# Performance work log

Measured on AMD Instinct MI355X. Metric: run time of the kernel, lower is better.

The kernel has to match this reference:

```python
import jax, jax.numpy as jnp
import numpy as np

GRID_SHAPE = (256, 256)  # SOM lattice dims -> M = 65536 nodes, ndim = 2
D = 32                   # input feature dim
B = 2048                 # batch size


def _make_grid_flat():
    # tf.meshgrid(indexing='ij') stacked on last axis, flattened to [1, M, ndim]
    mesh = np.stack(np.meshgrid(*[np.arange(s) for s in GRID_SHAPE], indexing='ij'), axis=-1)
    g = mesh.reshape(1, -1, len(GRID_SHAPE)).astype(np.float32)
    # faithful to source: per-axis mean (reduce_mean axis=1), GLOBAL std (reduce_std, no axis)
    g = (g - g.mean(axis=1, keepdims=True)) / g.std()
    return jnp.asarray(g)


def setup_inputs() -> dict:
    key = jax.random.key(0)
    k1, k2 = jax.random.split(key)
    grid_flat = _make_grid_flat()                                  # [1, M, 2]
    M = grid_flat.shape[1]
    w = jax.random.normal(k1, (1, M, D), dtype=jnp.float32)        # codebook (non-trainable in source)
    x = jax.random.normal(k2, (B, D), dtype=jnp.float32)
    return {"x": x, "grid_flat": grid_flat, "w": w}


def reference(x, grid_flat, w):
    # squared L2 distance from each input to every codebook vector.
    # computed here without materializing the [B, M, D] broadcast.
    wm = w[0]  # [M, D]
    d2 = (jnp.sum(x * x, axis=1, keepdims=True)
          - 2.0 * (x @ wm.T)
          + jnp.sum(wm * wm, axis=1)[None, :])  # [B, M]
    # source: top_k(-|d2|, k=1); d2 >= 0 so abs is identity, kept for fidelity
    _, idx = jax.lax.top_k(-jnp.abs(d2), 1)  # idx: [B, 1]
    bmu = grid_flat[0][idx[:, 0]]            # gather winning grid coords -> [B, 2]
    return bmu
```

## Files before the change

kernel.cpp:

```cpp
#include <hip/hip_runtime.h>
#include <stdint.h>

#define D       32
#define B       2048
#define M       65536
#define STRIPS  1024
#define CHUNKS  4
#define CHCOLS  (B / CHUNKS)
#define NTILES  (CHCOLS / 16)
#define SGROUPS 32
#define SPERG   (STRIPS / SGROUPS)

typedef _Float16 half8 __attribute__((ext_vector_type(8)));
typedef float    floatx4 __attribute__((ext_vector_type(4)));


__global__ void som_wnorm_kernel(const float* __restrict__ w,
                                 float* __restrict__ wnorm) {
    int t   = blockIdx.x * blockDim.x + threadIdx.x;
    int row = t >> 2;
    int j   = t & 3;
    const float4* p = (const float4*)(w + (size_t)row * D) + j * 2;
    float4 a = p[0];
    float4 b4 = p[1];
    float s = a.x * a.x + a.y * a.y + a.z * a.z + a.w * a.w
            + b4.x * b4.x + b4.y * b4.y + b4.z * b4.z + b4.w * b4.w;
    s += __shfl_xor(s, 1);
    s += __shfl_xor(s, 2);
    if (j == 0) wnorm[row] = 0.5f * s;
}

__global__ void split_x_kernel(const float* __restrict__ x,
                               _Float16* __restrict__ xh,
                               _Float16* __restrict__ xl) {
    int i = blockIdx.x * blockDim.x + threadIdx.x;
    float v = x[i];
    _Float16 h = (_Float16)v;
    xh[i] = h;
    xl[i] = (_Float16)(v - (float)h);
}

__global__ __launch_bounds__(256, 4)
void som_mfma_kernel(const float* __restrict__ w,
                     const float* __restrict__ wnorm,
                     const _Float16* __restrict__ x_hi,
                     const _Float16* __restrict__ x_lo,
                     uint64_t* __restrict__ pkeys) {
    const int s    = blockIdx.x;
    const int wv   = threadIdx.x >> 6;
    const int lane = threadIdx.x & 63;
    const int q    = lane >> 4;
    const int j    = lane & 15;

    half8 a_hi[4], a_lo[4];
#pragma unroll
    for (int t = 0; t < 4; t++) {
        const float* wp = w + (size_t)(s * 64 + t * 16 + j) * D + q * 8;
        float4 f0 = ((const float4*)wp)[0];
        float4 f1 = ((const float4*)wp)[1];
        float f[8] = {f0.x, f0.y, f0.z, f0.w, f1.x, f1.y, f1.z, f1.w};
#pragma unroll
        for (int k = 0; k < 8; k++) {
            _Float16 h = (_Float16)f[k];
            a_hi[t][k] = h;
            a_lo[t][k] = (_Float16)(f[k] - (float)h);
        }
    }

    float wn[4][4];
#pragma unroll
    for (int t = 0; t < 4; t++)
#pragma unroll
        for (int r = 0; r < 4; r++)
            wn[t][r] = wnorm[s * 64 + t * 16 + q * 4 + r];

    uint64_t* pk = pkeys + (size_t)s * B;

    for (int it = 0; it < NTILES; it++) {
        const int nb  = wv * CHCOLS + it * 16;
        const int col = nb + j;
        const half8 bh = *(const half8*)(x_hi + (size_t)col * D + q * 8);
        const half8 bl = *(const half8*)(x_lo + (size_t)col * D + q * 8);

        floatx4 acc[4];
#pragma unroll
        for (int t = 0; t < 4; t++)
            acc[t] = __builtin_amdgcn_mfma_f32_16x16x32_f16(
                a_lo[t], bh, (floatx4){0.f, 0.f, 0.f, 0.f}, 0, 0, 0);
#pragma unroll
        for (int t = 0; t < 4; t++)
            acc[t] = __builtin_amdgcn_mfma_f32_16x16x32_f16(a_hi[t], bl, acc[t], 0, 0, 0);
#pragma unroll
        for (int t = 0; t < 4; t++)
            acc[t] = __builtin_amdgcn_mfma_f32_16x16x32_f16(a_hi[t], bh, acc[t], 0, 0, 0);

        float best = -3.4e38f;
        int   brow = 0;
#pragma unroll
        for (int t = 0; t < 4; t++)
#pragma unroll
            for (int r = 0; r < 4; r++) {
                float sc  = acc[t][r] - wn[t][r];
                int   row = s * 64 + t * 16 + q * 4 + r;
                if (sc > best) { best = sc; brow = row; }
            }

        uint32_t u = __float_as_uint(best);
        u ^= (uint32_t)((int32_t)u >> 31) | 0x80000000u;
        uint64_t key = ((uint64_t)u << 32) | (uint64_t)(~(uint32_t)brow);

        uint64_t o;
        o = (uint64_t)__shfl_xor((long long)key, 16); if (o > key) key = o;
        o = (uint64_t)__shfl_xor((long long)key, 32); if (o > key) key = o;

        if (lane < 16) pk[col] = key;
    }
}

__global__ void som_reduce1_kernel(const uint64_t* __restrict__ pkeys,
                                   uint64_t* __restrict__ s2) {
    const int col = blockIdx.x * 256 + threadIdx.x;
    const int sg  = blockIdx.y;
    uint64_t best = 0;
#pragma unroll 8
    for (int t = 0; t < SPERG; t++) {
        uint64_t k = pkeys[(size_t)(sg * SPERG + t) * B + col];
        if (k > best) best = k;
    }
    s2[(size_t)sg * B + col] = best;
}

__global__ void som_reduce2_kernel(const uint64_t* __restrict__ s2,
                                   const float* __restrict__ grid_flat,
                                   float* __restrict__ out) {
    const int b = blockIdx.x * 256 + threadIdx.x;
    uint64_t best = 0;
#pragma unroll
    for (int sg = 0; sg < SGROUPS; sg++) {
        uint64_t k = s2[(size_t)sg * B + b];
        if (k > best) best = k;
    }
    uint32_t idx = ~(uint32_t)best;
    float2 g = ((const float2*)grid_flat)[idx];
    ((float2*)out)[b] = g;
}

#define MTILES  128
#define MTILE   (M / MTILES)
#define BTILE   256

__global__ __launch_bounds__(BTILE, 8)
void som_score_kernel(const float* __restrict__ x,
                      const float* __restrict__ w,
                      const float* __restrict__ wnorm,
                      float* __restrict__ pscore,
                      int*   __restrict__ pidx) {
    const int bt = blockIdx.x;
    const int mt = blockIdx.y;
    const int b  = bt * BTILE + threadIdx.x;

    float xr[D];
    const float4* xp = (const float4*)(x + (size_t)b * D);
#pragma unroll
    for (int i = 0; i < D / 4; i++) {
        float4 v = xp[i];
        xr[4 * i + 0] = v.x; xr[4 * i + 1] = v.y;
        xr[4 * i + 2] = v.z; xr[4 * i + 3] = v.w;
    }

    const int m0 = mt * MTILE;
    float best = -3.0e38f;
    int   bidx = m0;
#pragma unroll 2
    for (int mm = 0; mm < MTILE; mm++) {
        const int m = m0 + mm;
        const float* __restrict__ wr = w + (size_t)m * D;
        float acc = 0.0f;
#pragma unroll
        for (int i = 0; i < D; i++) acc = fmaf(xr[i], wr[i], acc);
        const float score = acc - wnorm[m];
        if (score > best) { best = score; bidx = m; }
    }
    pscore[(size_t)b * MTILES + mt] = best;
    pidx  [(size_t)b * MTILES + mt] = bidx;
}

__global__ void som_reduce_kernel(const float* __restrict__ pscore,
                                  const int*   __restrict__ pidx,
                                  const float* __restrict__ grid_flat,
                                  float* __restrict__ out) {
    const int b = blockIdx.x * blockDim.x + threadIdx.x;
    const float* ps = pscore + (size_t)b * MTILES;
    const int*   pi = pidx   + (size_t)b * MTILES;
    float best = -3.0e38f;
    int   bidx = 0x7fffffff;
#pragma unroll 4
    for (int t = 0; t < MTILES; t++) {
        const float s  = ps[t];
        const int   id = pi[t];
        if (s > best || (s == best && id < bidx)) { best = s; bidx = id; }
    }
    const float2 g = ((const float2*)grid_flat)[bidx];
    ((float2*)out)[b] = g;
}

extern "C" void kernel_launch(void* const* d_in, const int* in_sizes, int n_in,
                              void* d_out, int out_size, void* d_ws, size_t ws_size,
                              hipStream_t stream) {
    const float* x         = (const float*)d_in[0];
    const float* grid_flat = (const float*)d_in[1];
    const float* w         = (const float*)d_in[2];
    float* out = (float*)d_out;

    char* ws = (char*)d_ws;
    const size_t XH_OFF   = 0;
    const size_t XL_OFF   = XH_OFF + (size_t)B * D * sizeof(_Float16);
    const size_t WN_OFF   = XL_OFF + (size_t)B * D * sizeof(_Float16);
    const size_t PK_OFF   = WN_OFF + (size_t)M * sizeof(float);
    const size_t S2_OFF   = PK_OFF + (size_t)STRIPS * B * sizeof(uint64_t);
    const size_t NEED     = S2_OFF + (size_t)SGROUPS * B * sizeof(uint64_t);

    if (ws_size >= NEED) {
        _Float16* x_hi  = (_Float16*)(ws + XH_OFF);
        _Float16* x_lo  = (_Float16*)(ws + XL_OFF);
        float*    wnorm = (float*)(ws + WN_OFF);
        uint64_t* pkeys = (uint64_t*)(ws + PK_OFF);
        uint64_t* s2    = (uint64_t*)(ws + S2_OFF);

        som_wnorm_kernel<<<(M * 4) / 256, 256, 0, stream>>>(w, wnorm);
        split_x_kernel<<<(B * D) / 256, 256, 0, stream>>>(x, x_hi, x_lo);
        som_mfma_kernel<<<STRIPS, 256, 0, stream>>>(w, wnorm, x_hi, x_lo, pkeys);
        som_reduce1_kernel<<<dim3(B / 256, SGROUPS), 256, 0, stream>>>(pkeys, s2);
        som_reduce2_kernel<<<B / 256, 256, 0, stream>>>(s2, grid_flat, out);
    } else {
        float* wnorm  = (float*)d_ws;
        float* pscore = wnorm + M;
        int*   pidx   = (int*)(pscore + (size_t)B * MTILES);

        som_wnorm_kernel<<<(M * 4) / 256, 256, 0, stream>>>(w, wnorm);
        dim3 grid1(B / BTILE, MTILES);
        som_score_kernel<<<grid1, BTILE, 0, stream>>>(x, w, wnorm, pscore, pidx);
        som_reduce_kernel<<<B / 256, 256, 0, stream>>>(pscore, pidx, grid_flat, out);
    }
}
```

Baseline: 111.5 us.

## Track only per-strip max score in MFMA loop and recompute winning row exactly

The MFMA kernel now keeps only the per-column maximum score of each 64-row strip as a 32-bit sortable value, dropping the argmax tracking and the 64-bit key. The wnorm bias is folded into the MFMA accumulator init, and the loop is unrolled by two. The reductions find the best strip per column, and a new final kernel rescores that strip's 64 rows in fp32 to pick the exact row before gathering grid coordinates. The wnorm and x-split kernels are also merged into one launch. This trims ALU work and partial-result traffic. The risk is that the strip chosen from the approximate scores may not hold the true fp32 argmax when scores nearly tie.

New measurement: 101.8 us. 1.09x faster.

```diff
diff --git a/kernel.cpp b/kernel.cpp
--- a/kernel.cpp
+++ b/kernel.cpp
@@ -14,6 +14,169 @@
 typedef _Float16 half8 __attribute__((ext_vector_type(8)));
 typedef float    floatx4 __attribute__((ext_vector_type(4)));
 
+
+__device__ __forceinline__ uint32_t f32_sortable(float f) {
+    uint32_t u = __float_as_uint(f);
+    u ^= (uint32_t)((int32_t)u >> 31) | 0x80000000u;
+    return u;
+}
+
+__global__ void som_prep_kernel(const float* __restrict__ w,
+                                const float* __restrict__ x,
+                                float* __restrict__ wnorm,
+                                _Float16* __restrict__ xh,
+                                _Float16* __restrict__ xl) {
+    if (blockIdx.x < (M * 4) / 256) {
+        int t   = blockIdx.x * 256 + threadIdx.x;
+        int row = t >> 2;
+        int j   = t & 3;
+        const float4* p = (const float4*)(w + (size_t)row * D) + j * 2;
+        float4 a = p[0];
+        float4 b4 = p[1];
+        float s = a.x * a.x + a.y * a.y + a.z * a.z + a.w * a.w
+                + b4.x * b4.x + b4.y * b4.y + b4.z * b4.z + b4.w * b4.w;
+        s += __shfl_xor(s, 1);
+        s += __shfl_xor(s, 2);
+        if (j == 0) wnorm[row] = 0.5f * s;
+    } else {
+        int i = (blockIdx.x - (M * 4) / 256) * 256 + threadIdx.x;
+        float v = x[i];
+        _Float16 h = (_Float16)v;
+        xh[i] = h;
+        xl[i] = (_Float16)(v - (float)h);
+    }
+}
+
+__global__ __launch_bounds__(256, 4)
+void som_mfma_kernel(const float* __restrict__ w,
+                     const float* __restrict__ wnorm,
+                     const _Float16* __restrict__ x_hi,
+                     const _Float16* __restrict__ x_lo,
+                     uint32_t* __restrict__ pmax) {
+    const int s    = blockIdx.x;
+    const int wv   = threadIdx.x >> 6;
+    const int lane = threadIdx.x & 63;
+    const int q    = lane >> 4;
+    const int j    = lane & 15;
+
+    half8 a_hi[4], a_lo[4];
+#pragma unroll
+    for (int t = 0; t < 4; t++) {
+        const float* wp = w + (size_t)(s * 64 + t * 16 + j) * D + q * 8;
+        float4 f0 = ((const float4*)wp)[0];
+        float4 f1 = ((const float4*)wp)[1];
+        float f[8] = {f0.x, f0.y, f0.z, f0.w, f1.x, f1.y, f1.z, f1.w};
+#pragma unroll
+        for (int k = 0; k < 8; k++) {
+            _Float16 h = (_Float16)f[k];
+            a_hi[t][k] = h;
+            a_lo[t][k] = (_Float16)(f[k] - (float)h);
+        }
+    }
+
+    floatx4 init[4];
+#pragma unroll
+    for (int t = 0; t < 4; t++)
+#pragma unroll
+        for (int r = 0; r < 4; r++)
+            init[t][r] = -wnorm[s * 64 + t * 16 + q * 4 + r];
+
+    uint32_t* pm = pmax + (size_t)s * B;
+
+#pragma unroll 2
+    for (int it = 0; it < NTILES; it++) {
+        const int col = wv * CHCOLS + it * 16 + j;
+        const half8 bh = *(const half8*)(x_hi + (size_t)col * D + q * 8);
+        const half8 bl = *(const half8*)(x_lo + (size_t)col * D + q * 8);
+
+        floatx4 acc[4];
+#pragma unroll
+        for (int t = 0; t < 4; t++)
+            acc[t] = __builtin_amdgcn_mfma_f32_16x16x32_f16(a_lo[t], bh, init[t], 0, 0, 0);
+#pragma unroll
+        for (int t = 0; t < 4; t++)
+            acc[t] = __builtin_amdgcn_mfma_f32_16x16x32_f16(a_hi[t], bl, acc[t], 0, 0, 0);
+#pragma unroll
+        for (int t = 0; t < 4; t++)
+            acc[t] = __builtin_amdgcn_mfma_f32_16x16x32_f16(a_hi[t], bh, acc[t], 0, 0, 0);
+
+        float b0 = fmaxf(fmaxf(acc[0][0], acc[0][1]), fmaxf(acc[0][2], acc[0][3]));
+        float b1 = fmaxf(fmaxf(acc[1][0], acc[1][1]), fmaxf(acc[1][2], acc[1][3]));
+        float b2 = fmaxf(fmaxf(acc[2][0], acc[2][1]), fmaxf(acc[2][2], acc[2][3]));
+        float b3 = fmaxf(fmaxf(acc[3][0], acc[3][1]), fmaxf(acc[3][2], acc[3][3]));
+        float best = fmaxf(fmaxf(b0, b1), fmaxf(b2, b3));
+
+        best = fmaxf(best, __shfl_xor(best, 16));
+        best = fmaxf(best, __shfl_xor(best, 32));
+
+        if (lane < 16) pm[col] = f32_sortable(best);
+    }
+}
+
+__global__ void som_reduce1_kernel(const uint32_t* __restrict__ pmax,
+                                   uint64_t* __restrict__ s2) {
+    const int col = blockIdx.x * 256 + threadIdx.x;
+    const int sg  = blockIdx.y;
+    uint32_t best = pmax[(size_t)(sg * SPERG) * B + col];
+    int bstrip = sg * SPERG;
+#pragma unroll 8
+    for (int t = 1; t < SPERG; t++) {
+        uint32_t u = pmax[(size_t)(sg * SPERG + t) * B + col];
+        if (u > best) { best = u; bstrip = sg * SPERG + t; }
+    }
+    s2[(size_t)sg * B + col] = ((uint64_t)best << 32) | (uint32_t)(~(uint32_t)bstrip);
+}
+
+__global__ __launch_bounds__(256)
+void som_final_kernel(const uint64_t* __restrict__ s2,
+                      const float* __restrict__ x,
+                      const float* __restrict__ w,
+                      const float* __restrict__ wnorm,
+                      const float* __restrict__ grid_flat,
+                      float* __restrict__ out) {
+    const int wv   = threadIdx.x >> 6;
+    const int lane = threadIdx.x & 63;
+    const int col  = blockIdx.x * 4 + wv;
+
+    uint64_t k = (lane < SGROUPS) ? s2[(size_t)lane * B + col] : 0ull;
+    {
+        uint64_t o;
+        o = (uint64_t)__shfl_xor((long long)k,  1); if (o > k) k = o;
+        o = (uint64_t)__shfl_xor((long long)k,  2); if (o > k) k = o;
+        o = (uint64_t)__shfl_xor((long long)k,  4); if (o > k) k = o;
+        o = (uint64_t)__shfl_xor((long long)k,  8); if (o > k) k = o;
+        o = (uint64_t)__shfl_xor((long long)k, 16); if (o > k) k = o;
+        o = (uint64_t)__shfl_xor((long long)k, 32); if (o > k) k = o;
+    }
+    const int strip = (int)(~(uint32_t)k);
+    const int row   = strip * 64 + lane;
+
+    const float* xc = x + (size_t)col * D;
+    const float* wr = w + (size_t)row * D;
+    float acc = 0.0f;
+#pragma unroll
+    for (int i = 0; i < D; i++) acc = fmaf(xc[i], wr[i], acc);
+    const float score = acc - wnorm[row];
+
+    uint64_t key = ((uint64_t)f32_sortable(score) << 32) | (uint32_t)(~(uint32_t)row);
+    {
+        uint64_t o;
+        o = (uint64_t)__shfl_xor((long long)key,  1); if (o > key) key = o;
+        o = (uint64_t)__shfl_xor((long long)key,  2); if (o > key) key = o;
+        o = (uint64_t)__shfl_xor((long long)key,  4); if (o > key) key = o;
+        o = (uint64_t)__shfl_xor((long long)key,  8); if (o > key) key = o;
+        o = (uint64_t)__shfl_xor((long long)key, 16); if (o > key) key = o;
+        o = (uint64_t)__shfl_xor((long long)key, 32); if (o > key) key = o;
+    }
+    if (lane == 0) {
+        const uint32_t idx = ~(uint32_t)key;
+        ((float2*)out)[col] = ((const float2*)grid_flat)[idx];
+    }
+}
+
+#define MTILES  128
+#define MTILE   (M / MTILES)
+#define BTILE   256
 
 __global__ void som_wnorm_kernel(const float* __restrict__ w,
                                  float* __restrict__ wnorm) {
@@ -29,125 +192,6 @@
     s += __shfl_xor(s, 2);
     if (j == 0) wnorm[row] = 0.5f * s;
 }
-
-__global__ void split_x_kernel(const float* __restrict__ x,
-                               _Float16* __restrict__ xh,
-                               _Float16* __restrict__ xl) {
-    int i = blockIdx.x * blockDim.x + threadIdx.x;
-    float v = x[i];
-    _Float16 h = (_Float16)v;
-    xh[i] = h;
-    xl[i] = (_Float16)(v - (float)h);
-}
-
-__global__ __launch_bounds__(256, 4)
-void som_mfma_kernel(const float* __restrict__ w,
-                     const float* __restrict__ wnorm,
-                     const _Float16* __restrict__ x_hi,
-                     const _Float16* __restrict__ x_lo,
-                     uint64_t* __restrict__ pkeys) {
-    const int s    = blockIdx.x;
-    const int wv   = threadIdx.x >> 6;
-    const int lane = threadIdx.x & 63;
-    const int q    = lane >> 4;
-    const int j    = lane & 15;
-
-    half8 a_hi[4], a_lo[4];
-#pragma unroll
-    for (int t = 0; t < 4; t++) {
-        const float* wp = w + (size_t)(s * 64 + t * 16 + j) * D + q * 8;
-        float4 f0 = ((const float4*)wp)[0];
-        float4 f1 = ((const float4*)wp)[1];
-        float f[8] = {f0.x, f0.y, f0.z, f0.w, f1.x, f1.y, f1.z, f1.w};
-#pragma unroll
-        for (int k = 0; k < 8; k++) {
-            _Float16 h = (_Float16)f[k];
-            a_hi[t][k] = h;
-            a_lo[t][k] = (_Float16)(f[k] - (float)h);
-        }
-    }
-
-    float wn[4][4];
-#pragma unroll
-    for (int t = 0; t < 4; t++)
-#pragma unroll
-        for (int r = 0; r < 4; r++)
-            wn[t][r] = wnorm[s * 64 + t * 16 + q * 4 + r];
-
-    uint64_t* pk = pkeys + (size_t)s * B;
-
-    for (int it = 0; it < NTILES; it++) {
-        const int nb  = wv * CHCOLS + it * 16;
-        const int col = nb + j;
-        const half8 bh = *(const half8*)(x_hi + (size_t)col * D + q * 8);
-        const half8 bl = *(const half8*)(x_lo + (size_t)col * D + q * 8);
-
-        floatx4 acc[4];
-#pragma unroll
-        for (int t = 0; t < 4; t++)
-            acc[t] = __builtin_amdgcn_mfma_f32_16x16x32_f16(
-                a_lo[t], bh, (floatx4){0.f, 0.f, 0.f, 0.f}, 0, 0, 0);
-#pragma unroll
-        for (int t = 0; t < 4; t++)
-            acc[t] = __builtin_amdgcn_mfma_f32_16x16x32_f16(a_hi[t], bl, acc[t], 0, 0, 0);
-#pragma unroll
-        for (int t = 0; t < 4; t++)
-            acc[t] = __builtin_amdgcn_mfma_f32_16x16x32_f16(a_hi[t], bh, acc[t], 0, 0, 0);
-
-        float best = -3.4e38f;
-        int   brow = 0;
-#pragma unroll
-        for (int t = 0; t < 4; t++)
-#pragma unroll
-            for (int r = 0; r < 4; r++) {
-                float sc  = acc[t][r] - wn[t][r];
-                int   row = s * 64 + t * 16 + q * 4 + r;
-                if (sc > best) { best = sc; brow = row; }
-            }
-
-        uint32_t u = __float_as_uint(best);
-        u ^= (uint32_t)((int32_t)u >> 31) | 0x80000000u;
-        uint64_t key = ((uint64_t)u << 32) | (uint64_t)(~(uint32_t)brow);
-
-        uint64_t o;
-        o = (uint64_t)__shfl_xor((long long)key, 16); if (o > key) key = o;
-        o = (uint64_t)__shfl_xor((long long)key, 32); if (o > key) key = o;
-
-        if (lane < 16) pk[col] = key;
-    }
-}
-
-__global__ void som_reduce1_kernel(const uint64_t* __restrict__ pkeys,
-                                   uint64_t* __restrict__ s2) {
-    const int col = blockIdx.x * 256 + threadIdx.x;
-    const int sg  = blockIdx.y;
-    uint64_t best = 0;
-#pragma unroll 8
-    for (int t = 0; t < SPERG; t++) {
-        uint64_t k = pkeys[(size_t)(sg * SPERG + t) * B + col];
-        if (k > best) best = k;
-    }
-    s2[(size_t)sg * B + col] = best;
-}
-
-__global__ void som_reduce2_kernel(const uint64_t* __restrict__ s2,
-                                   const float* __restrict__ grid_flat,
-                                   float* __restrict__ out) {
-    const int b = blockIdx.x * 256 + threadIdx.x;
-    uint64_t best = 0;
-#pragma unroll
-    for (int sg = 0; sg < SGROUPS; sg++) {
-        uint64_t k = s2[(size_t)sg * B + b];
-        if (k > best) best = k;
-    }
-    uint32_t idx = ~(uint32_t)best;
-    float2 g = ((const float2*)grid_flat)[idx];
-    ((float2*)out)[b] = g;
-}
-
-#define MTILES  128
-#define MTILE   (M / MTILES)
-#define BTILE   256
 
 __global__ __launch_bounds__(BTILE, 8)
 void som_score_kernel(const float* __restrict__ x,
@@ -200,8 +244,7 @@
         const int   id = pi[t];
         if (s > best || (s == best && id < bidx)) { best = s; bidx = id; }
     }
-    const float2 g = ((const float2*)grid_flat)[bidx];
-    ((float2*)out)[b] = g;
+    ((float2*)out)[b] = ((const float2*)grid_flat)[bidx];
 }
 
 extern "C" void kernel_launch(void* const* d_in, const int* in_sizes, int n_in,
@@ -213,25 +256,25 @@
     float* out = (float*)d_out;
 
     char* ws = (char*)d_ws;
-    const size_t XH_OFF   = 0;
-    const size_t XL_OFF   = XH_OFF + (size_t)B * D * sizeof(_Float16);
-    const size_t WN_OFF   = XL_OFF + (size_t)B * D * sizeof(_Float16);
-    const size_t PK_OFF   = WN_OFF + (size_t)M * sizeof(float);
-    const size_t S2_OFF   = PK_OFF + (size_t)STRIPS * B * sizeof(uint64_t);
-    const size_t NEED     = S2_OFF + (size_t)SGROUPS * B * sizeof(uint64_t);
+    const size_t XH_OFF = 0;
+    const size_t XL_OFF = XH_OFF + (size_t)B * D * sizeof(_Float16);
+    const size_t WN_OFF = XL_OFF + (size_t)B * D * sizeof(_Float16);
+    const size_t PM_OFF = WN_OFF + (size_t)M * sizeof(float);
+    const size_t S2_OFF = PM_OFF + (size_t)STRIPS * B * sizeof(uint32_t);
+    const size_t NEED   = S2_OFF + (size_t)SGROUPS * B * sizeof(uint64_t);
 
     if (ws_size >= NEED) {
         _Float16* x_hi  = (_Float16*)(ws + XH_OFF);
         _Float16* x_lo  = (_Float16*)(ws + XL_OFF);
         float*    wnorm = (float*)(ws + WN_OFF);
-        uint64_t* pkeys = (uint64_t*)(ws + PK_OFF);
+        uint32_t* pmax  = (uint32_t*)(ws + PM_OFF);
         uint64_t* s2    = (uint64_t*)(ws + S2_OFF);
 
-        som_wnorm_kernel<<<(M * 4) / 256, 256, 0, stream>>>(w, wnorm);
-        split_x_kernel<<<(B * D) / 256, 256, 0, stream>>>(x, x_hi, x_lo);
-        som_mfma_kernel<<<STRIPS, 256, 0, stream>>>(w, wnorm, x_hi, x_lo, pkeys);
-        som_reduce1_kernel<<<dim3(B / 256, SGROUPS), 256, 0, stream>>>(pkeys, s2);
-        som_reduce2_kernel<<<B / 256, 256, 0, stream>>>(s2, grid_flat, out);
+        som_prep_kernel<<<(M * 4) / 256 + (B * D) / 256, 256, 0, stream>>>(
+            w, x, wnorm, x_hi, x_lo);
+        som_mfma_kernel<<<STRIPS, 256, 0, stream>>>(w, wnorm, x_hi, x_lo, pmax);
+        som_reduce1_kernel<<<dim3(B / 256, SGROUPS), 256, 0, stream>>>(pmax, s2);
+        som_final_kernel<<<B / 4, 256, 0, stream>>>(s2, x, w, wnorm, grid_flat, out);
     } else {
         float* wnorm  = (float*)d_ws;
         float* pscore = wnorm + M;
```
